# Performance work log

Measured on AMD Instinct MI355X. Metric: run time of the kernel, lower is better.

Reference implementation:

```python
import jax, jax.numpy as jnp
import numpy as np

NUM_USERS = 50000
NUM_FOODS = 20000
USER_FEAT_DIM = 256
FOOD_FEAT_DIM = 256
EMBED_DIM = 128
NUM_LAYERS = 3
NUM_HEADS = 4
THRESHOLD = 0.3
E_UF = 600000  # user->food interactions; symmetrized to 2*E_UF directed edges


def setup_inputs() -> dict:
    key = jax.random.key(0)
    ks = jax.random.split(key, 12)
    user_feat = jax.random.normal(ks[0], (NUM_USERS, USER_FEAT_DIM), jnp.float32)
    food_feat = jax.random.normal(ks[1], (NUM_FOODS, FOOD_FEAT_DIM), jnp.float32)
    # bipartite edges in global index space, symmetrized (both directions)
    u = jax.random.randint(ks[2], (E_UF,), 0, NUM_USERS)
    f = jax.random.randint(ks[3], (E_UF,), 0, NUM_FOODS) + NUM_USERS
    edge_index = jnp.stack([jnp.concatenate([u, f]), jnp.concatenate([f, u])]).astype(jnp.int64)
    s = 0.02
    W_user = jax.random.normal(ks[4], (USER_FEAT_DIM, EMBED_DIM), jnp.float32) * s
    b_user = jnp.zeros((EMBED_DIM,), jnp.float32)
    W_food = jax.random.normal(ks[5], (FOOD_FEAT_DIM, EMBED_DIM), jnp.float32) * s
    b_food = jnp.zeros((EMBED_DIM,), jnp.float32)
    Wq = jax.random.normal(ks[6], (EMBED_DIM, EMBED_DIM), jnp.float32) * s
    Wk = jax.random.normal(ks[7], (EMBED_DIM, EMBED_DIM), jnp.float32) * s
    channel_weights = jnp.zeros((2,), jnp.float32)  # StructurePooling fusion weights
    user_embed = jax.random.normal(ks[8], (NUM_USERS, EMBED_DIM), jnp.float32) * 0.1
    item_embed = jax.random.normal(ks[9], (NUM_FOODS, EMBED_DIM), jnp.float32) * 0.1
    return {"user_feat": user_feat, "food_feat": food_feat, "edge_index": edge_index,
            "W_user": W_user, "b_user": b_user, "W_food": W_food, "b_food": b_food,
            "Wq": Wq, "Wk": Wk, "channel_weights": channel_weights,
            "user_embed": user_embed, "item_embed": item_embed}


def reference(user_feat, food_feat, edge_index, W_user, b_user, W_food, b_food,
              Wq, Wk, channel_weights, user_embed, item_embed):
    N = NUM_USERS + NUM_FOODS
    Dh = EMBED_DIM // NUM_HEADS
    # feature projections + relu
    user_emb = jax.nn.relu(user_feat @ W_user + b_user)   # [U, D]
    food_emb = jax.nn.relu(food_feat @ W_food + b_food)   # [F, D]
    row, col = edge_index[0], edge_index[1]
    # graph generator: per-edge multi-head cosine similarity between user/food endpoints
    u_idx = jnp.where(row < NUM_USERS, row, col)
    f_idx = jnp.where(row < NUM_USERS, col, row) - NUM_USERS
    q = (user_emb[u_idx] @ Wq).reshape(-1, NUM_HEADS, Dh)  # [E, H, Dh]
    k = (food_emb[f_idx] @ Wk).reshape(-1, NUM_HEADS, Dh)
    eps = 1e-8
    sim = (q * k).sum(-1) / (jnp.linalg.norm(q, axis=-1) * jnp.linalg.norm(k, axis=-1) + eps)
    mask_feature = (sim.mean(-1) > THRESHOLD).astype(jnp.float32)  # [E]
    # structure pooling fusion of [all-ones, feature mask]
    w = jax.nn.softmax(channel_weights)
    fused = w[0] * 1.0 + w[1] * mask_feature
    edge_mask = (fused > 0.5).astype(jnp.float32)
    # LightGCN: symmetric-normalized propagation on the masked graph
    deg = jnp.maximum(jax.ops.segment_sum(edge_mask, row, num_segments=N), 1.0)
    norm = edge_mask / jnp.sqrt(deg[row] * deg[col])       # [E]
    x0 = jnp.concatenate([user_embed, item_embed], axis=0)  # [N, D]
    x = x0
    acc = x0
    for _ in range(NUM_LAYERS):
        x = jax.ops.segment_sum(norm[:, None] * x[col], row, num_segments=N)
        acc = acc + x
    out = acc / float(NUM_LAYERS + 1)
    return (out[:NUM_USERS], out[NUM_USERS:], user_embed, item_embed)
```

## Files before the change

kernel.cpp:

```cpp
#include <hip/hip_runtime.h>
#include <cstdint>

#define U_NUM 50000
#define F_NUM 20000
#define N_NUM 70000
#define D_EMB 128
#define THRESH 0.3f

typedef _Float16 half8 __attribute__((ext_vector_type(8)));
typedef float f32x4 __attribute__((ext_vector_type(4)));
typedef unsigned short u16x8 __attribute__((ext_vector_type(8)));

#define NBT_U ((U_NUM + 63) / 64)
#define NBT_F ((F_NUM + 63) / 64)

__device__ __forceinline__ void gl_lds16(const void* g, void* l)
{
    __builtin_amdgcn_global_load_lds(
        (const __attribute__((address_space(1))) unsigned int*)g,
        (__attribute__((address_space(3))) unsigned int*)l, 16, 0, 0);
}

__global__ void presplit_zero(const float* __restrict__ Wu, const float* __restrict__ Wf,
                              const float* __restrict__ Wq, const float* __restrict__ Wk,
                              unsigned short* __restrict__ dst,
                              int* __restrict__ cnt, int* __restrict__ cursor)
{
    int i = blockIdx.x * 256 + threadIdx.x;
    if (i < N_NUM) { cnt[i] = 0; cursor[i] = 0; }
    if (i >= 98304) return;
    float a; size_t d; int pstride;
    if (i < 32768) {
        int n = i >> 8, k = i & 255;
        a = Wu[k * 128 + n]; d = (size_t)n * 256 + k; pstride = 32768;
    } else if (i < 65536) {
        int j = i - 32768; int n = j >> 8, k = j & 255;
        a = Wf[k * 128 + n]; d = 65536 + (size_t)n * 256 + k; pstride = 32768;
    } else if (i < 81920) {
        int j = i - 65536; int n = j >> 7, k = j & 127;
        a = Wq[k * 128 + n]; d = 131072 + (size_t)n * 128 + k; pstride = 16384;
    } else {
        int j = i - 81920; int n = j >> 7, k = j & 127;
        a = Wk[k * 128 + n]; d = 163840 + (size_t)n * 128 + k; pstride = 16384;
    }
    _Float16 c1 = (_Float16)a;
    float r = a - (float)c1;
    _Float16 c2 = (_Float16)r;
    dst[d]           = __builtin_bit_cast(unsigned short, c1);
    dst[d + pstride] = __builtin_bit_cast(unsigned short, c2);
}

__device__ __forceinline__ void split2v(const f32x4 x0, const f32x4 x1,
                                        half8& h, half8& lo)
{
    float v[8] = {x0[0], x0[1], x0[2], x0[3], x1[0], x1[1], x1[2], x1[3]};
#pragma unroll
    for (int i = 0; i < 8; i++) {
        _Float16 c1 = (_Float16)v[i];
        h[i] = c1;
        lo[i] = (_Float16)(v[i] - (float)c1);
    }
}

__global__ __launch_bounds__(256, 2)
void fused_gemm(const float* __restrict__ uf, const float* __restrict__ ff,
                const unsigned short* __restrict__ Wsp,
                const float* __restrict__ bu, const float* __restrict__ bfo,
                float* __restrict__ Qo, unsigned short* __restrict__ QKh)
{
    __shared__ char lds[81920];

    const int bid = blockIdx.x;
    const bool isU = bid < NBT_U;
    const int rt = isU ? bid : bid - NBT_U;
    const int Mloc = isU ? U_NUM : F_NUM;
    const int combBase = isU ? 0 : U_NUM;
    const float* A  = isU ? uf : ff;
    const float* b1 = isU ? bu : bfo;
    const unsigned short* W1 = Wsp + (isU ? 0 : 65536);
    const unsigned short* W2 = Wsp + (isU ? 131072 : 163840);

    const int tid = threadIdx.x;
    const int w  = tid >> 6;
    const int l  = tid & 63;
    const int lm = l & 15;
    const int lq = l >> 4;

    auto stageA = [&](int b, int kc) {
#pragma unroll
        for (int j = 0; j < 2; ++j) {
            int off = j * 4096 + tid * 16;
            int row = off >> 7;
            int ch  = (off & 127) >> 4;
            int gch = ch ^ (row & 7);
            int gr  = min(rt * 64 + row, Mloc - 1);
            const float* src = A + (size_t)gr * 256 + kc * 32 + gch * 4;
            gl_lds16(src, lds + b * 8192 + j * 4096 + w * 1024);
        }
    };
    auto stageW1 = [&](int b, int kc) {
#pragma unroll
        for (int j = 0; j < 4; ++j) {
            int off = w * 4096 + j * 1024 + l * 16;
            int p   = off >> 13;
            int n   = (off & 8191) >> 6;
            int ch  = (off & 63) >> 4;
            int gch = ch ^ ((n >> 1) & 3);
            const unsigned short* src = W1 + (size_t)p * 32768 + (size_t)n * 256 + kc * 32 + gch * 8;
            gl_lds16(src, lds + 16384 + b * 16384 + w * 4096 + j * 1024);
        }
    };
    auto stageW2 = [&](int b, int kc) {
#pragma unroll
        for (int j = 0; j < 4; ++j) {
            int off = w * 4096 + j * 1024 + l * 16;
            int p   = off >> 13;
            int n   = (off & 8191) >> 6;
            int ch  = (off & 63) >> 4;
            int gch = ch ^ ((n >> 1) & 3);
            const unsigned short* src = W2 + (size_t)p * 16384 + (size_t)n * 128 + kc * 32 + gch * 8;
            gl_lds16(src, lds + 16384 + b * 16384 + w * 4096 + j * 1024);
        }
    };

    stageA(0, 0); stageW1(0, 0);
    __syncthreads();

    f32x4 acc1[8];
#pragma unroll
    for (int j = 0; j < 8; j++) acc1[j] = (f32x4)0.f;

    int buf = 0;
#pragma unroll
    for (int kc = 0; kc < 8; ++kc) {
        if (kc < 7) { stageA(buf ^ 1, kc + 1); stageW1(buf ^ 1, kc + 1); }

        half8 ah, al;
        {
            int lr = w * 16 + lm;
            int r7 = lr & 7;
            const float* basep = (const float*)(lds + buf * 8192 + lr * 128);
            f32x4 x0 = *(const f32x4*)(basep + ((((lq * 2)    ) ^ r7) << 2));
            f32x4 x1 = *(const f32x4*)(basep + ((((lq * 2) + 1) ^ r7) << 2));
            split2v(x0, x1, ah, al);
        }
#pragma unroll
        for (int cb = 0; cb < 8; ++cb) {
            int n = cb * 16 + lm;
            int wc = lq ^ ((n >> 1) & 3);
            const char* wbase = lds + 16384 + buf * 16384;
            half8 bh = *(const half8*)(wbase + n * 64 + wc * 16);
            half8 bl = *(const half8*)(wbase + 8192 + n * 64 + wc * 16);
            acc1[cb] = __builtin_amdgcn_mfma_f32_16x16x32_f16(al, bh, acc1[cb], 0, 0, 0);
            acc1[cb] = __builtin_amdgcn_mfma_f32_16x16x32_f16(ah, bl, acc1[cb], 0, 0, 0);
            acc1[cb] = __builtin_amdgcn_mfma_f32_16x16x32_f16(ah, bh, acc1[cb], 0, 0, 0);
        }
        __syncthreads();
        buf ^= 1;
    }

    float* EW = (float*)(lds + 49152 + w * 8192);
#pragma unroll
    for (int cb = 0; cb < 8; ++cb) {
        const int col = cb * 16 + lm;
        const float bb = b1[col];
#pragma unroll
        for (int rg = 0; rg < 4; ++rg) {
            const int row = lq * 4 + rg;
            float e = fmaxf(acc1[cb][rg] + bb, 0.f);
            EW[row * 128 + ((((col >> 2) ^ (row & 7)) << 2) | (col & 3))] = e;
        }
    }

    f32x4 acc2[8];
#pragma unroll
    for (int j = 0; j < 8; j++) acc2[j] = (f32x4)0.f;

    stageW2(0, 0);
    __syncthreads();
    buf = 0;
#pragma unroll
    for (int kc = 0; kc < 4; ++kc) {
        if (kc < 3) stageW2(buf ^ 1, kc + 1);

        half8 ah, al;
        {
            const int row = lm;
            const int r7 = row & 7;
            const int c0 = kc * 8 + lq * 2;
            f32x4 x0 = *(const f32x4*)(EW + row * 128 + (((c0    ) ^ r7) << 2));
            f32x4 x1 = *(const f32x4*)(EW + row * 128 + (((c0 + 1) ^ r7) << 2));
            split2v(x0, x1, ah, al);
        }
#pragma unroll
        for (int cb = 0; cb < 8; ++cb) {
            int n = cb * 16 + lm;
            int wc = lq ^ ((n >> 1) & 3);
            const char* wbase = lds + 16384 + buf * 16384;
            half8 bh = *(const half8*)(wbase + n * 64 + wc * 16);
            half8 bl = *(const half8*)(wbase + 8192 + n * 64 + wc * 16);
            acc2[cb] = __builtin_amdgcn_mfma_f32_16x16x32_f16(al, bh, acc2[cb], 0, 0, 0);
            acc2[cb] = __builtin_amdgcn_mfma_f32_16x16x32_f16(ah, bl, acc2[cb], 0, 0, 0);
            acc2[cb] = __builtin_amdgcn_mfma_f32_16x16x32_f16(ah, bh, acc2[cb], 0, 0, 0);
        }
        __syncthreads();
        buf ^= 1;
    }

#pragma unroll
    for (int cb = 0; cb < 8; ++cb) {
        const int col = cb * 16 + lm;
#pragma unroll
        for (int rg = 0; rg < 4; ++rg) {
            int lr = rt * 64 + w * 16 + lq * 4 + rg;
            if (lr < Mloc) {
                size_t rr = (size_t)(combBase + lr);
                float v = acc2[cb][rg];
                Qo[rr * 128 + col] = v;
                QKh[rr * 128 + col] = __builtin_bit_cast(unsigned short, (_Float16)v);
            }
        }
    }
}

__global__ __launch_bounds__(256)
void edge_kernel(const int* __restrict__ ei, int Edir,
                 const unsigned short* __restrict__ QKh, const float* __restrict__ QKf,
                 const float* __restrict__ cwts,
                 float* __restrict__ maskf, int* __restrict__ cnt, int Eund)
{
    int gid = blockIdx.x * 256 + threadIdx.x;
    int e = gid >> 3;
    if (e >= Eund) return;
    int sub = gid & 7;
    int row = ei[e];
    int col = ei[Edir + e];
    row = min(max(row, 0), N_NUM - 1);
    col = min(max(col, 0), N_NUM - 1);
    int u  = (row < U_NUM) ? row : col;
    int fg = (row < U_NUM) ? col : row;
    u = min(max(u, 0), U_NUM - 1);
    int f = min(max(fg - U_NUM, 0), F_NUM - 1);
    const size_t qrow = (size_t)u * D_EMB;
    const size_t krow = (size_t)(U_NUM + f) * D_EMB;

    const unsigned short* qh = QKh + qrow + sub * 16;
    const unsigned short* kh = QKh + krow + sub * 16;
    u16x8 qa = *(const u16x8*)(qh);
    u16x8 qb = *(const u16x8*)(qh + 8);
    u16x8 ka = *(const u16x8*)(kh);
    u16x8 kb = *(const u16x8*)(kh + 8);
    float dot = 0.f, qq = 0.f, kk = 0.f;
#pragma unroll
    for (int i = 0; i < 8; i++) {
        float qv = (float)__builtin_bit_cast(_Float16, (unsigned short)qa[i]);
        float kv = (float)__builtin_bit_cast(_Float16, (unsigned short)ka[i]);
        dot += qv * kv; qq += qv * qv; kk += kv * kv;
    }
#pragma unroll
    for (int i = 0; i < 8; i++) {
        float qv = (float)__builtin_bit_cast(_Float16, (unsigned short)qb[i]);
        float kv = (float)__builtin_bit_cast(_Float16, (unsigned short)kb[i]);
        dot += qv * kv; qq += qv * qv; kk += kv * kv;
    }
    dot += __shfl_xor(dot, 1);
    qq  += __shfl_xor(qq, 1);
    kk  += __shfl_xor(kk, 1);
    float denom = sqrtf(qq) * sqrtf(kk) + 1e-8f;
    float sim = dot / denom;
    float s = sim + __shfl_xor(sim, 2);
    s += __shfl_xor(s, 4);
    float mean = s * 0.25f;

    if (fabsf(mean - THRESH) < 0.03f) {
        const float4* qp = (const float4*)(QKf + qrow + sub * 16);
        const float4* kp = (const float4*)(QKf + krow + sub * 16);
        float dot2 = 0.f, qq2 = 0.f, kk2 = 0.f;
#pragma unroll
        for (int i = 0; i < 4; i++) {
            float4 a = qp[i]; float4 b = kp[i];
            dot2 += a.x * b.x + a.y * b.y + a.z * b.z + a.w * b.w;
            qq2  += a.x * a.x + a.y * a.y + a.z * a.z + a.w * a.w;
            kk2  += b.x * b.x + b.y * b.y + b.z * b.z + b.w * b.w;
        }
        dot2 += __shfl_xor(dot2, 1);
        qq2  += __shfl_xor(qq2, 1);
        kk2  += __shfl_xor(kk2, 1);
        float denom2 = sqrtf(qq2) * sqrtf(kk2) + 1e-8f;
        float sim2 = dot2 / denom2;
        float s2 = sim2 + __shfl_xor(sim2, 2);
        s2 += __shfl_xor(s2, 4);
        mean = s2 * 0.25f;
    }

    float mf = (mean > THRESH) ? 1.f : 0.f;
    float cw0 = cwts[0], cw1 = cwts[1];
    float mx = fmaxf(cw0, cw1);
    float e0 = expf(cw0 - mx), e1 = expf(cw1 - mx);
    float inv = 1.f / (e0 + e1);
    float fused = e0 * inv + (e1 * inv) * mf;
    float em = (fused > 0.5f) ? 1.f : 0.f;

    if (sub == 0) {
        maskf[e] = em;
        if (em != 0.f) {
            atomicAdd(&cnt[row], 1);
            atomicAdd(&cnt[col], 1);
        }
    }
}

__global__ void scan_part(const int* __restrict__ cnt, int* __restrict__ part, int n)
{
    __shared__ int sd[256];
    int b = blockIdx.x, t = threadIdx.x;
    int base = b * 1024;
    int s = 0;
#pragma unroll
    for (int j = 0; j < 4; j++) {
        int idx = base + t + j * 256;
        if (idx < n) s += cnt[idx];
    }
    sd[t] = s; __syncthreads();
    for (int d = 128; d > 0; d >>= 1) {
        if (t < d) sd[t] += sd[t + d];
        __syncthreads();
    }
    if (t == 0) part[b] = sd[0];
}

__global__ void scan_small(int* part, int nb)
{
    __shared__ int sd[256];
    int t = threadIdx.x;
    sd[t] = (t < nb) ? part[t] : 0;
    __syncthreads();
    for (int d = 1; d < 256; d <<= 1) {
        int x = (t >= d) ? sd[t - d] : 0;
        __syncthreads();
        sd[t] += x;
        __syncthreads();
    }
    if (t < nb) part[t] = (t > 0) ? sd[t - 1] : 0;
}

__global__ void scan_final(const int* __restrict__ cnt, const int* __restrict__ part,
                           int* __restrict__ offs, int n)
{
    __shared__ int sd[256];
    int b = blockIdx.x, t = threadIdx.x;
    int base = b * 1024 + t * 4;
    int v[4]; int s = 0;
#pragma unroll
    for (int j = 0; j < 4; j++) {
        int idx = base + j;
        v[j] = (idx < n) ? cnt[idx] : 0;
        s += v[j];
    }
    sd[t] = s; __syncthreads();
    for (int d = 1; d < 256; d <<= 1) {
        int x = (t >= d) ? sd[t - d] : 0;
        __syncthreads();
        sd[t] += x;
        __syncthreads();
    }
    int prefix = part[b] + ((t > 0) ? sd[t - 1] : 0);
#pragma unroll
    for (int j = 0; j < 4; j++) {
        int idx = base + j;
        if (idx < n) offs[idx] = prefix;
        prefix += v[j];
    }
}

__global__ void scatter_kernel(const int* __restrict__ ei, int Edir,
                               const float* __restrict__ maskf,
                               const int* __restrict__ cnt, const int* __restrict__ offs,
                               int* __restrict__ cursor,
                               int* __restrict__ cnbr, float* __restrict__ cwA, int Eund)
{
    int e = blockIdx.x * 256 + threadIdx.x;
    if (e >= Eund) return;
    if (maskf[e] == 0.f) return;
    int row = ei[e], col = ei[Edir + e];
    row = min(max(row, 0), N_NUM - 1);
    col = min(max(col, 0), N_NUM - 1);
    float w = 1.0f / sqrtf((float)cnt[row] * (float)cnt[col]);
    int p1 = offs[row] + atomicAdd(&cursor[row], 1);
    cnbr[p1] = col; cwA[p1] = w;
    int p2 = offs[col] + atomicAdd(&cursor[col], 1);
    cnbr[p2] = row; cwA[p2] = w;
}

template<int MODE>
__global__ __launch_bounds__(256)
void prop(const int* __restrict__ offs, const int* __restrict__ cnt,
          const int* __restrict__ cnbr, const float* __restrict__ cwA,
          const float* __restrict__ xin,
          const float* __restrict__ ue, const float* __restrict__ ie,
          const float* __restrict__ x1b, float* __restrict__ xout,
          float* __restrict__ tail)
{
    int wid = (blockIdx.x << 2) + (threadIdx.x >> 6);
    if (wid >= N_NUM) return;
    int lane = threadIdx.x & 63;
    int num = cnt[wid];
    if (MODE != 2 && num == 0) return;
    int start = (num > 0) ? offs[wid] : 0;
    float ax = 0.f, ay = 0.f;

    auto srcp = [&](int c) -> const float* {
        if (MODE == 0)
            return (c < U_NUM) ? (ue + (size_t)c * D_EMB) : (ie + (size_t)(c - U_NUM) * D_EMB);
        else
            return xin + (size_t)c * D_EMB;
    };

    int j = 0;
    for (; j + 4 <= num; j += 4) {
        int c0i = cnbr[start + j],     c1i = cnbr[start + j + 1];
        int c2i = cnbr[start + j + 2], c3i = cnbr[start + j + 3];
        float w0 = cwA[start + j],     w1 = cwA[start + j + 1];
        float w2 = cwA[start + j + 2], w3 = cwA[start + j + 3];
        float2 v0 = *(const float2*)(srcp(c0i) + lane * 2);
        float2 v1 = *(const float2*)(srcp(c1i) + lane * 2);
        float2 v2 = *(const float2*)(srcp(c2i) + lane * 2);
        float2 v3 = *(const float2*)(srcp(c3i) + lane * 2);
        ax += w0 * v0.x; ay += w0 * v0.y;
        ax += w1 * v1.x; ay += w1 * v1.y;
        ax += w2 * v2.x; ay += w2 * v2.y;
        ax += w3 * v3.x; ay += w3 * v3.y;
    }
    for (; j < num; ++j) {
        int c = cnbr[start + j]; float w = cwA[start + j];
        float2 v = *(const float2*)(srcp(c) + lane * 2);
        ax += w * v.x; ay += w * v.y;
    }

    size_t o = (size_t)wid * D_EMB + lane * 2;
    if (MODE == 2) {
        const float* x0p = (wid < U_NUM) ? (ue + (size_t)wid * D_EMB)
                                         : (ie + (size_t)(wid - U_NUM) * D_EMB);
        float2 x0v = *(const float2*)(x0p + lane * 2);
        *(float2*)(tail + o) = x0v;
        float ox, oy;
        if (num == 0) {
            ox = x0v.x * 0.25f; oy = x0v.y * 0.25f;
        } else {
            float2 x1v = *(const float2*)(x1b + o);
            float2 x2v = *(const float2*)(xin + o);
            ox = ((x0v.x + x1v.x) + x2v.x + ax) * 0.25f;
            oy = ((x0v.y + x1v.y) + x2v.y + ay) * 0.25f;
        }
        *(float2*)(xout + o) = make_float2(ox, oy);
    } else {
        *(float2*)(xout + o) = make_float2(ax, ay);
    }
}

extern "C" void kernel_launch(void* const* d_in, const int* in_sizes, int n_in,
                              void* d_out, int out_size, void* d_ws, size_t ws_size,
                              hipStream_t stream)
{
    const float* user_feat  = (const float*)d_in[0];
    const float* food_feat  = (const float*)d_in[1];
    const int*   ei         = (const int*)d_in[2];
    const float* W_user     = (const float*)d_in[3];
    const float* b_user     = (const float*)d_in[4];
    const float* W_food     = (const float*)d_in[5];
    const float* b_food     = (const float*)d_in[6];
    const float* Wq         = (const float*)d_in[7];
    const float* Wk         = (const float*)d_in[8];
    const float* cwts       = (const float*)d_in[9];
    const float* user_embed = (const float*)d_in[10];
    const float* item_embed = (const float*)d_in[11];

    const int Edir = in_sizes[2] / 2;
    const int Eund = Edir / 2;

    char* ws = (char*)d_ws;
    size_t off = 0;
    auto alloc = [&](size_t nb) { size_t o = off; off += (nb + 255) & ~(size_t)255; return o; };

    float* Q     = (float*)(ws + alloc((size_t)N_NUM * D_EMB * 4));
    float* xB    = (float*)(ws + alloc((size_t)N_NUM * D_EMB * 4));
    unsigned short* QKh = (unsigned short*)(ws + alloc((size_t)N_NUM * D_EMB * 2));
    float* maskf = (float*)(ws + alloc((size_t)Eund * 4));
    int*   cnt   = (int*)  (ws + alloc((size_t)N_NUM * 4));
    int*   offs  = (int*)  (ws + alloc((size_t)N_NUM * 4));
    int*   cursor= (int*)  (ws + alloc((size_t)N_NUM * 4));
    int*   cnbr  = (int*)  (ws + alloc((size_t)Edir * 4));
    float* cwA   = (float*)(ws + alloc((size_t)Edir * 4));
    int*   part  = (int*)  (ws + alloc((size_t)256 * 4));
    unsigned short* Wsp = (unsigned short*)(ws + alloc((size_t)196608 * 2));
    (void)ws_size; (void)n_in; (void)out_size;

    float* xA = Q;

    presplit_zero<<<384, 256, 0, stream>>>(W_user, W_food, Wq, Wk, Wsp, cnt, cursor);

    fused_gemm<<<NBT_U + NBT_F, 256, 0, stream>>>(user_feat, food_feat, Wsp,
                                                  b_user, b_food, Q, QKh);

    edge_kernel<<<(Eund * 8 + 255) / 256, 256, 0, stream>>>(ei, Edir, QKh, Q, cwts,
                                                            maskf, cnt, Eund);

    int nb = (N_NUM + 1023) / 1024;
    scan_part <<<nb, 256, 0, stream>>>(cnt, part, N_NUM);
    scan_small<<<1, 256, 0, stream>>>(part, nb);
    scan_final<<<nb, 256, 0, stream>>>(cnt, part, offs, N_NUM);

    scatter_kernel<<<(Eund + 255) / 256, 256, 0, stream>>>(ei, Edir, maskf, cnt, offs,
                                                           cursor, cnbr, cwA, Eund);

    int pb = (N_NUM + 3) / 4;
    float* tail = (float*)d_out + (size_t)N_NUM * D_EMB;
    prop<0><<<pb, 256, 0, stream>>>(offs, cnt, cnbr, cwA, nullptr, user_embed, item_embed,
                                    nullptr, xB, nullptr);
    prop<1><<<pb, 256, 0, stream>>>(offs, cnt, cnbr, cwA, xB, user_embed, item_embed,
                                    nullptr, xA, nullptr);
    prop<2><<<pb, 256, 0, stream>>>(offs, cnt, cnbr, cwA, xA, user_embed, item_embed,
                                    xB, (float*)d_out, tail);
}
```

Measured before the change: 129.3 us.

## Shrink GEMM row tile to 32 and split output columns across waves

The fused projection GEMM now handles 32 rows per block instead of 64. Each wave computes a 16-row by 64-column quadrant instead of a 16-row by 128-column slab. The whole 32x256 A tile is loaded into LDS once up front rather than double-buffered per K chunk, and the intermediate ReLU tile is reused in place of A for the second GEMM. LDS drops to 64KB and the grid doubles, aiming for more blocks in flight and fewer accumulator registers. In exchange, the weights are staged twice as often per output row.

```diff
diff --git a/kernel.cpp b/kernel.cpp
--- a/kernel.cpp
+++ b/kernel.cpp
@@ -11,8 +11,8 @@
 typedef float f32x4 __attribute__((ext_vector_type(4)));
 typedef unsigned short u16x8 __attribute__((ext_vector_type(8)));
 
-#define NBT_U ((U_NUM + 63) / 64)
-#define NBT_F ((F_NUM + 63) / 64)
+#define NBT_U ((U_NUM + 31) / 32)
+#define NBT_F ((F_NUM + 31) / 32)
 
 __device__ __forceinline__ void gl_lds16(const void* g, void* l)
 {
@@ -68,7 +68,7 @@
                 const float* __restrict__ bu, const float* __restrict__ bfo,
                 float* __restrict__ Qo, unsigned short* __restrict__ QKh)
 {
-    __shared__ char lds[81920];
+    __shared__ char lds[65536];
 
     const int bid = blockIdx.x;
     const bool isU = bid < NBT_U;
@@ -85,19 +85,22 @@
     const int l  = tid & 63;
     const int lm = l & 15;
     const int lq = l >> 4;
-
-    auto stageA = [&](int b, int kc) {
-#pragma unroll
-        for (int j = 0; j < 2; ++j) {
+    const int rh  = w & 1;
+    const int chf = w >> 1;
+
+    {
+#pragma unroll
+        for (int j = 0; j < 8; ++j) {
             int off = j * 4096 + tid * 16;
-            int row = off >> 7;
-            int ch  = (off & 127) >> 4;
+            int row = off >> 10;
+            int ch  = (off & 1023) >> 4;
             int gch = ch ^ (row & 7);
-            int gr  = min(rt * 64 + row, Mloc - 1);
-            const float* src = A + (size_t)gr * 256 + kc * 32 + gch * 4;
-            gl_lds16(src, lds + b * 8192 + j * 4096 + w * 1024);
-        }
-    };
+            int gr  = min(rt * 32 + row, Mloc - 1);
+            const float* src = A + (size_t)gr * 256 + gch * 4;
+            gl_lds16(src, lds + j * 4096 + w * 1024);
+        }
+    }
+
     auto stageW1 = [&](int b, int kc) {
 #pragma unroll
         for (int j = 0; j < 4; ++j) {
@@ -107,7 +110,7 @@
             int ch  = (off & 63) >> 4;
             int gch = ch ^ ((n >> 1) & 3);
             const unsigned short* src = W1 + (size_t)p * 32768 + (size_t)n * 256 + kc * 32 + gch * 8;
-            gl_lds16(src, lds + 16384 + b * 16384 + w * 4096 + j * 1024);
+            gl_lds16(src, lds + 32768 + b * 16384 + w * 4096 + j * 1024);
         }
     };
     auto stageW2 = [&](int b, int kc) {
@@ -119,36 +122,37 @@
             int ch  = (off & 63) >> 4;
             int gch = ch ^ ((n >> 1) & 3);
             const unsigned short* src = W2 + (size_t)p * 16384 + (size_t)n * 128 + kc * 32 + gch * 8;
-            gl_lds16(src, lds + 16384 + b * 16384 + w * 4096 + j * 1024);
+            gl_lds16(src, lds + 32768 + b * 16384 + w * 4096 + j * 1024);
         }
     };
 
-    stageA(0, 0); stageW1(0, 0);
+    stageW1(0, 0);
     __syncthreads();
 
-    f32x4 acc1[8];
-#pragma unroll
-    for (int j = 0; j < 8; j++) acc1[j] = (f32x4)0.f;
+    f32x4 acc1[4];
+#pragma unroll
+    for (int j = 0; j < 4; j++) acc1[j] = (f32x4)0.f;
 
     int buf = 0;
 #pragma unroll
     for (int kc = 0; kc < 8; ++kc) {
-        if (kc < 7) { stageA(buf ^ 1, kc + 1); stageW1(buf ^ 1, kc + 1); }
+        if (kc < 7) stageW1(buf ^ 1, kc + 1);
 
         half8 ah, al;
         {
-            int lr = w * 16 + lm;
-            int r7 = lr & 7;
-            const float* basep = (const float*)(lds + buf * 8192 + lr * 128);
-            f32x4 x0 = *(const f32x4*)(basep + ((((lq * 2)    ) ^ r7) << 2));
-            f32x4 x1 = *(const f32x4*)(basep + ((((lq * 2) + 1) ^ r7) << 2));
+            int row = rh * 16 + lm;
+            int r7 = row & 7;
+            int c0 = kc * 8 + lq * 2;
+            const float* basep = (const float*)(lds + row * 1024);
+            f32x4 x0 = *(const f32x4*)(basep + (((c0    ) ^ r7) << 2));
+            f32x4 x1 = *(const f32x4*)(basep + (((c0 + 1) ^ r7) << 2));
             split2v(x0, x1, ah, al);
         }
 #pragma unroll
-        for (int cb = 0; cb < 8; ++cb) {
-            int n = cb * 16 + lm;
+        for (int cb = 0; cb < 4; ++cb) {
+            int n = chf * 64 + cb * 16 + lm;
             int wc = lq ^ ((n >> 1) & 3);
-            const char* wbase = lds + 16384 + buf * 16384;
+            const char* wbase = lds + 32768 + buf * 16384;
             half8 bh = *(const half8*)(wbase + n * 64 + wc * 16);
             half8 bl = *(const half8*)(wbase + 8192 + n * 64 + wc * 16);
             acc1[cb] = __builtin_amdgcn_mfma_f32_16x16x32_f16(al, bh, acc1[cb], 0, 0, 0);
@@ -159,25 +163,27 @@
         buf ^= 1;
     }
 
-    float* EW = (float*)(lds + 49152 + w * 8192);
-#pragma unroll
-    for (int cb = 0; cb < 8; ++cb) {
-        const int col = cb * 16 + lm;
-        const float bb = b1[col];
-#pragma unroll
-        for (int rg = 0; rg < 4; ++rg) {
-            const int row = lq * 4 + rg;
-            float e = fmaxf(acc1[cb][rg] + bb, 0.f);
-            EW[row * 128 + ((((col >> 2) ^ (row & 7)) << 2) | (col & 3))] = e;
-        }
-    }
-
-    f32x4 acc2[8];
-#pragma unroll
-    for (int j = 0; j < 8; j++) acc2[j] = (f32x4)0.f;
-
     stageW2(0, 0);
+    {
+        float* E = (float*)lds;
+#pragma unroll
+        for (int cb = 0; cb < 4; ++cb) {
+            const int col = chf * 64 + cb * 16 + lm;
+            const float bb = b1[col];
+#pragma unroll
+            for (int rg = 0; rg < 4; ++rg) {
+                const int row = rh * 16 + lq * 4 + rg;
+                float e = fmaxf(acc1[cb][rg] + bb, 0.f);
+                E[row * 128 + ((((col >> 2) ^ (row & 7)) << 2) | (col & 3))] = e;
+            }
+        }
+    }
     __syncthreads();
+
+    f32x4 acc2[4];
+#pragma unroll
+    for (int j = 0; j < 4; j++) acc2[j] = (f32x4)0.f;
+
     buf = 0;
 #pragma unroll
     for (int kc = 0; kc < 4; ++kc) {
@@ -185,18 +191,19 @@
 
         half8 ah, al;
         {
-            const int row = lm;
+            const int row = rh * 16 + lm;
             const int r7 = row & 7;
             const int c0 = kc * 8 + lq * 2;
-            f32x4 x0 = *(const f32x4*)(EW + row * 128 + (((c0    ) ^ r7) << 2));
-            f32x4 x1 = *(const f32x4*)(EW + row * 128 + (((c0 + 1) ^ r7) << 2));
+            const float* E = (const float*)lds;
+            f32x4 x0 = *(const f32x4*)(E + row * 128 + (((c0    ) ^ r7) << 2));
+            f32x4 x1 = *(const f32x4*)(E + row * 128 + (((c0 + 1) ^ r7) << 2));
             split2v(x0, x1, ah, al);
         }
 #pragma unroll
-        for (int cb = 0; cb < 8; ++cb) {
-            int n = cb * 16 + lm;
+        for (int cb = 0; cb < 4; ++cb) {
+            int n = chf * 64 + cb * 16 + lm;
             int wc = lq ^ ((n >> 1) & 3);
-            const char* wbase = lds + 16384 + buf * 16384;
+            const char* wbase = lds + 32768 + buf * 16384;
             half8 bh = *(const half8*)(wbase + n * 64 + wc * 16);
             half8 bl = *(const half8*)(wbase + 8192 + n * 64 + wc * 16);
             acc2[cb] = __builtin_amdgcn_mfma_f32_16x16x32_f16(al, bh, acc2[cb], 0, 0, 0);
@@ -208,11 +215,11 @@
     }
 
 #pragma unroll
-    for (int cb = 0; cb < 8; ++cb) {
-        const int col = cb * 16 + lm;
+    for (int cb = 0; cb < 4; ++cb) {
+        const int col = chf * 64 + cb * 16 + lm;
 #pragma unroll
         for (int rg = 0; rg < 4; ++rg) {
-            int lr = rt * 64 + w * 16 + lq * 4 + rg;
+            int lr = rt * 32 + rh * 16 + lq * 4 + rg;
             if (lr < Mloc) {
                 size_t rr = (size_t)(combBase + lr);
                 float v = acc2[cb][rg];
```

Result: slower. 133.3 us (+3.0%).

## Use single fp16 GEMMs and recheck near-threshold edges exactly in fp32

Applied to the files above, without the earlier changes.

Replaces the split-fp16 (three MFMA) emulation of fp32 in both projection GEMMs with a single fp16 MFMA per tile, halving weight staging and LDS use. Launch bounds are raised so more blocks fit per CU. The fp32 Q/K output and the in-kernel fp32 recheck are removed. Edges whose fp16 similarity falls within a band of the threshold are pushed to a list, and a new kernel recomputes them from raw features in fp32 and fixes the mask and degree counts. This risks mismatches if fp16 error exceeds the band, and adds per-edge recompute cost proportional to the band population.

```diff
diff --git a/kernel.cpp b/kernel.cpp
--- a/kernel.cpp
+++ b/kernel.cpp
@@ -6,6 +6,7 @@
 #define N_NUM 70000
 #define D_EMB 128
 #define THRESH 0.3f
+#define BAND 0.02f
 
 typedef _Float16 half8 __attribute__((ext_vector_type(8)));
 typedef float f32x4 __attribute__((ext_vector_type(4)));
@@ -24,51 +25,37 @@
 __global__ void presplit_zero(const float* __restrict__ Wu, const float* __restrict__ Wf,
                               const float* __restrict__ Wq, const float* __restrict__ Wk,
                               unsigned short* __restrict__ dst,
-                              int* __restrict__ cnt, int* __restrict__ cursor)
+                              int* __restrict__ cnt, int* __restrict__ cursor,
+                              int* __restrict__ bcount)
 {
     int i = blockIdx.x * 256 + threadIdx.x;
+    if (i == 0) *bcount = 0;
     if (i < N_NUM) { cnt[i] = 0; cursor[i] = 0; }
     if (i >= 98304) return;
-    float a; size_t d; int pstride;
+    float a; size_t d;
     if (i < 32768) {
         int n = i >> 8, k = i & 255;
-        a = Wu[k * 128 + n]; d = (size_t)n * 256 + k; pstride = 32768;
+        a = Wu[k * 128 + n]; d = (size_t)n * 256 + k;
     } else if (i < 65536) {
         int j = i - 32768; int n = j >> 8, k = j & 255;
-        a = Wf[k * 128 + n]; d = 65536 + (size_t)n * 256 + k; pstride = 32768;
+        a = Wf[k * 128 + n]; d = 32768 + (size_t)n * 256 + k;
     } else if (i < 81920) {
         int j = i - 65536; int n = j >> 7, k = j & 127;
-        a = Wq[k * 128 + n]; d = 131072 + (size_t)n * 128 + k; pstride = 16384;
+        a = Wq[k * 128 + n]; d = 65536 + (size_t)n * 128 + k;
     } else {
         int j = i - 81920; int n = j >> 7, k = j & 127;
-        a = Wk[k * 128 + n]; d = 163840 + (size_t)n * 128 + k; pstride = 16384;
-    }
-    _Float16 c1 = (_Float16)a;
-    float r = a - (float)c1;
-    _Float16 c2 = (_Float16)r;
-    dst[d]           = __builtin_bit_cast(unsigned short, c1);
-    dst[d + pstride] = __builtin_bit_cast(unsigned short, c2);
-}
-
-__device__ __forceinline__ void split2v(const f32x4 x0, const f32x4 x1,
-                                        half8& h, half8& lo)
-{
-    float v[8] = {x0[0], x0[1], x0[2], x0[3], x1[0], x1[1], x1[2], x1[3]};
-#pragma unroll
-    for (int i = 0; i < 8; i++) {
-        _Float16 c1 = (_Float16)v[i];
-        h[i] = c1;
-        lo[i] = (_Float16)(v[i] - (float)c1);
-    }
-}
-
-__global__ __launch_bounds__(256, 2)
+        a = Wk[k * 128 + n]; d = 81920 + (size_t)n * 128 + k;
+    }
+    dst[d] = __builtin_bit_cast(unsigned short, (_Float16)a);
+}
+
+__global__ __launch_bounds__(256, 3)
 void fused_gemm(const float* __restrict__ uf, const float* __restrict__ ff,
                 const unsigned short* __restrict__ Wsp,
                 const float* __restrict__ bu, const float* __restrict__ bfo,
-                float* __restrict__ Qo, unsigned short* __restrict__ QKh)
-{
-    __shared__ char lds[81920];
+                unsigned short* __restrict__ QKh)
+{
+    __shared__ char lds[49152];
 
     const int bid = blockIdx.x;
     const bool isU = bid < NBT_U;
@@ -77,8 +64,8 @@
     const int combBase = isU ? 0 : U_NUM;
     const float* A  = isU ? uf : ff;
     const float* b1 = isU ? bu : bfo;
-    const unsigned short* W1 = Wsp + (isU ? 0 : 65536);
-    const unsigned short* W2 = Wsp + (isU ? 131072 : 163840);
+    const unsigned short* W1 = Wsp + (isU ? 0 : 32768);
+    const unsigned short* W2 = Wsp + (isU ? 65536 : 81920);
 
     const int tid = threadIdx.x;
     const int w  = tid >> 6;
@@ -99,31 +86,56 @@
         }
     };
     auto stageW1 = [&](int b, int kc) {
-#pragma unroll
-        for (int j = 0; j < 4; ++j) {
-            int off = w * 4096 + j * 1024 + l * 16;
-            int p   = off >> 13;
-            int n   = (off & 8191) >> 6;
+        {
+            int off = tid * 16;
+        }
+#pragma unroll
+        for (int j = 0; j < 2; ++j) {
+            int off = j * 4096 + tid * 16;
+            int n   = off >> 6;
             int ch  = (off & 63) >> 4;
             int gch = ch ^ ((n >> 1) & 3);
-            const unsigned short* src = W1 + (size_t)p * 32768 + (size_t)n * 256 + kc * 32 + gch * 8;
-            gl_lds16(src, lds + 16384 + b * 16384 + w * 4096 + j * 1024);
+            const unsigned short* src = W1 + (size_t)n * 256 + kc * 32 + gch * 8;
+            gl_lds16(src, lds + 16384 + b * 4096 + j * 4096 + w * 1024);
         }
     };
     auto stageW2 = [&](int b, int kc) {
 #pragma unroll
-        for (int j = 0; j < 4; ++j) {
-            int off = w * 4096 + j * 1024 + l * 16;
-            int p   = off >> 13;
-            int n   = (off & 8191) >> 6;
+        for (int j = 0; j < 2; ++j) {
+            int off = j * 4096 + tid * 16;
+            int n   = off >> 6;
             int ch  = (off & 63) >> 4;
             int gch = ch ^ ((n >> 1) & 3);
-            const unsigned short* src = W2 + (size_t)p * 16384 + (size_t)n * 128 + kc * 32 + gch * 8;
-            gl_lds16(src, lds + 16384 + b * 16384 + w * 4096 + j * 1024);
+            const unsigned short* src = W2 + (size_t)n * 128 + kc * 32 + gch * 8;
+            gl_lds16(src, lds + 16384 + b * 4096 + j * 4096 + w * 1024);
         }
     };
 
-    stageA(0, 0); stageW1(0, 0);
+    (void)stageW1; (void)stageW2;
+    auto stW1 = [&](int b, int kc) {
+#pragma unroll
+        for (int j = 0; j < 2; ++j) {
+            int off = j * 4096 + tid * 16;
+            int n   = off >> 6;
+            int ch  = (off & 63) >> 4;
+            int gch = ch ^ ((n >> 1) & 3);
+            const unsigned short* src = W1 + (size_t)n * 256 + kc * 32 + gch * 8;
+            gl_lds16(src, lds + 16384 + b * 8192 + off - (off & 15));
+        }
+    };
+    auto stW2 = [&](int b, int kc) {
+#pragma unroll
+        for (int j = 0; j < 2; ++j) {
+            int off = j * 4096 + tid * 16;
+            int n   = off >> 6;
+            int ch  = (off & 63) >> 4;
+            int gch = ch ^ ((n >> 1) & 3);
+            const unsigned short* src = W2 + (size_t)n * 128 + kc * 32 + gch * 8;
+            gl_lds16(src, lds + 16384 + b * 8192 + off - (off & 15));
+        }
+    };
+
+    stageA(0, 0); stW1(0, 0);
     __syncthreads();
 
     f32x4 acc1[8];
@@ -133,74 +145,69 @@
     int buf = 0;
 #pragma unroll
     for (int kc = 0; kc < 8; ++kc) {
-        if (kc < 7) { stageA(buf ^ 1, kc + 1); stageW1(buf ^ 1, kc + 1); }
-
-        half8 ah, al;
+        if (kc < 7) { stageA(buf ^ 1, kc + 1); stW1(buf ^ 1, kc + 1); }
+
+        half8 ah;
         {
             int lr = w * 16 + lm;
             int r7 = lr & 7;
             const float* basep = (const float*)(lds + buf * 8192 + lr * 128);
             f32x4 x0 = *(const f32x4*)(basep + ((((lq * 2)    ) ^ r7) << 2));
             f32x4 x1 = *(const f32x4*)(basep + ((((lq * 2) + 1) ^ r7) << 2));
-            split2v(x0, x1, ah, al);
+            float v[8] = {x0[0], x0[1], x0[2], x0[3], x1[0], x1[1], x1[2], x1[3]};
+#pragma unroll
+            for (int i = 0; i < 8; i++) ah[i] = (_Float16)v[i];
         }
 #pragma unroll
         for (int cb = 0; cb < 8; ++cb) {
             int n = cb * 16 + lm;
             int wc = lq ^ ((n >> 1) & 3);
-            const char* wbase = lds + 16384 + buf * 16384;
-            half8 bh = *(const half8*)(wbase + n * 64 + wc * 16);
-            half8 bl = *(const half8*)(wbase + 8192 + n * 64 + wc * 16);
-            acc1[cb] = __builtin_amdgcn_mfma_f32_16x16x32_f16(al, bh, acc1[cb], 0, 0, 0);
-            acc1[cb] = __builtin_amdgcn_mfma_f32_16x16x32_f16(ah, bl, acc1[cb], 0, 0, 0);
+            half8 bh = *(const half8*)(lds + 16384 + buf * 8192 + n * 64 + wc * 16);
             acc1[cb] = __builtin_amdgcn_mfma_f32_16x16x32_f16(ah, bh, acc1[cb], 0, 0, 0);
         }
         __syncthreads();
         buf ^= 1;
     }
 
-    float* EW = (float*)(lds + 49152 + w * 8192);
-#pragma unroll
-    for (int cb = 0; cb < 8; ++cb) {
-        const int col = cb * 16 + lm;
-        const float bb = b1[col];
-#pragma unroll
-        for (int rg = 0; rg < 4; ++rg) {
-            const int row = lq * 4 + rg;
-            float e = fmaxf(acc1[cb][rg] + bb, 0.f);
-            EW[row * 128 + ((((col >> 2) ^ (row & 7)) << 2) | (col & 3))] = e;
-        }
-    }
+    stW2(0, 0);
+    {
+        unsigned short* E = (unsigned short*)(lds + 32768);
+#pragma unroll
+        for (int cb = 0; cb < 8; ++cb) {
+            const int col = cb * 16 + lm;
+            const float bb = b1[col];
+#pragma unroll
+            for (int rg = 0; rg < 4; ++rg) {
+                const int row = w * 16 + lq * 4 + rg;
+                float e = fmaxf(acc1[cb][rg] + bb, 0.f);
+                int chn = (col >> 3) ^ (row & 7);
+                E[row * 128 + chn * 8 + (col & 7)] = __builtin_bit_cast(unsigned short, (_Float16)e);
+            }
+        }
+    }
+    __syncthreads();
 
     f32x4 acc2[8];
 #pragma unroll
     for (int j = 0; j < 8; j++) acc2[j] = (f32x4)0.f;
 
-    stageW2(0, 0);
-    __syncthreads();
     buf = 0;
 #pragma unroll
     for (int kc = 0; kc < 4; ++kc) {
-        if (kc < 3) stageW2(buf ^ 1, kc + 1);
-
-        half8 ah, al;
+        if (kc < 3) stW2(buf ^ 1, kc + 1);
+
+        half8 ah;
         {
-            const int row = lm;
+            const int row = w * 16 + lm;
             const int r7 = row & 7;
-            const int c0 = kc * 8 + lq * 2;
-            f32x4 x0 = *(const f32x4*)(EW + row * 128 + (((c0    ) ^ r7) << 2));
-            f32x4 x1 = *(const f32x4*)(EW + row * 128 + (((c0 + 1) ^ r7) << 2));
-            split2v(x0, x1, ah, al);
+            const int c0 = (kc * 4 + lq) ^ r7;
+            ah = *(const half8*)((const unsigned short*)(lds + 32768) + row * 128 + c0 * 8);
         }
 #pragma unroll
         for (int cb = 0; cb < 8; ++cb) {
             int n = cb * 16 + lm;
             int wc = lq ^ ((n >> 1) & 3);
-            const char* wbase = lds + 16384 + buf * 16384;
-            half8 bh = *(const half8*)(wbase + n * 64 + wc * 16);
-            half8 bl = *(const half8*)(wbase + 8192 + n * 64 + wc * 16);
-            acc2[cb] = __builtin_amdgcn_mfma_f32_16x16x32_f16(al, bh, acc2[cb], 0, 0, 0);
-            acc2[cb] = __builtin_amdgcn_mfma_f32_16x16x32_f16(ah, bl, acc2[cb], 0, 0, 0);
+            half8 bh = *(const half8*)(lds + 16384 + buf * 8192 + n * 64 + wc * 16);
             acc2[cb] = __builtin_amdgcn_mfma_f32_16x16x32_f16(ah, bh, acc2[cb], 0, 0, 0);
         }
         __syncthreads();
@@ -215,9 +222,7 @@
             int lr = rt * 64 + w * 16 + lq * 4 + rg;
             if (lr < Mloc) {
                 size_t rr = (size_t)(combBase + lr);
-                float v = acc2[cb][rg];
-                Qo[rr * 128 + col] = v;
-                QKh[rr * 128 + col] = __builtin_bit_cast(unsigned short, (_Float16)v);
+                QKh[rr * 128 + col] = __builtin_bit_cast(unsigned short, (_Float16)acc2[cb][rg]);
             }
         }
     }
@@ -225,9 +230,10 @@
 
 __global__ __launch_bounds__(256)
 void edge_kernel(const int* __restrict__ ei, int Edir,
-                 const unsigned short* __restrict__ QKh, const float* __restrict__ QKf,
+                 const unsigned short* __restrict__ QKh,
                  const float* __restrict__ cwts,
-                 float* __restrict__ maskf, int* __restrict__ cnt, int Eund)
+                 float* __restrict__ maskf, int* __restrict__ cnt,
+                 int* __restrict__ blist, int* __restrict__ bcount, int Eund)
 {
     int gid = blockIdx.x * 256 + threadIdx.x;
     int e = gid >> 3;
@@ -272,27 +278,6 @@
     s += __shfl_xor(s, 4);
     float mean = s * 0.25f;
 
-    if (fabsf(mean - THRESH) < 0.03f) {
-        const float4* qp = (const float4*)(QKf + qrow + sub * 16);
-        const float4* kp = (const float4*)(QKf + krow + sub * 16);
-        float dot2 = 0.f, qq2 = 0.f, kk2 = 0.f;
-#pragma unroll
-        for (int i = 0; i < 4; i++) {
-            float4 a = qp[i]; float4 b = kp[i];
-            dot2 += a.x * b.x + a.y * b.y + a.z * b.z + a.w * b.w;
-            qq2  += a.x * a.x + a.y * a.y + a.z * a.z + a.w * a.w;
-            kk2  += b.x * b.x + b.y * b.y + b.z * b.z + b.w * b.w;
-        }
-        dot2 += __shfl_xor(dot2, 1);
-        qq2  += __shfl_xor(qq2, 1);
-        kk2  += __shfl_xor(kk2, 1);
-        float denom2 = sqrtf(qq2) * sqrtf(kk2) + 1e-8f;
-        float sim2 = dot2 / denom2;
-        float s2 = sim2 + __shfl_xor(sim2, 2);
-        s2 += __shfl_xor(s2, 4);
-        mean = s2 * 0.25f;
-    }
-
     float mf = (mean > THRESH) ? 1.f : 0.f;
     float cw0 = cwts[0], cw1 = cwts[1];
     float mx = fmaxf(cw0, cw1);
@@ -306,6 +291,109 @@
         if (em != 0.f) {
             atomicAdd(&cnt[row], 1);
             atomicAdd(&cnt[col], 1);
+        }
+        if (fabsf(mean - THRESH) < BAND) {
+            int p = atomicAdd(bcount, 1);
+            blist[p] = e;
+        }
+    }
+}
+
+__global__ __launch_bounds__(256)
+void recheck_kernel(const int* __restrict__ ei, int Edir,
+                    const int* __restrict__ blist, const int* __restrict__ bcount,
+                    const float* __restrict__ uf, const float* __restrict__ ff,
+                    const float* __restrict__ Wu, const float* __restrict__ bu,
+                    const float* __restrict__ Wf, const float* __restrict__ bfo,
+                    const float* __restrict__ Wq, const float* __restrict__ Wk,
+                    const float* __restrict__ cwts,
+                    float* __restrict__ maskf, int* __restrict__ cnt)
+{
+    __shared__ float Esh[4][128];
+    const int w = threadIdx.x >> 6;
+    const int l = threadIdx.x & 63;
+    const int nwaves = gridDim.x * 4;
+    int widx = blockIdx.x * 4 + w;
+    const int total = *bcount;
+
+    for (int i = widx; i < total; i += nwaves) {
+        int e = blist[i];
+        int row = ei[e], col = ei[Edir + e];
+        row = min(max(row, 0), N_NUM - 1);
+        col = min(max(col, 0), N_NUM - 1);
+        int u  = (row < U_NUM) ? row : col;
+        int fg = (row < U_NUM) ? col : row;
+        u = min(max(u, 0), U_NUM - 1);
+        int f = min(max(fg - U_NUM, 0), F_NUM - 1);
+
+        float q0, q1, k0v, k1v;
+        {
+            const float* a = uf + (size_t)u * 256;
+            float e0 = 0.f, e1 = 0.f;
+            for (int k = 0; k < 256; ++k) {
+                float av = a[k];
+                e0 += av * Wu[k * 128 + l];
+                e1 += av * Wu[k * 128 + 64 + l];
+            }
+            e0 = fmaxf(e0 + bu[l], 0.f);
+            e1 = fmaxf(e1 + bu[64 + l], 0.f);
+            Esh[w][l] = e0; Esh[w][64 + l] = e1;
+            float s0 = 0.f, s1 = 0.f;
+            for (int k = 0; k < 128; ++k) {
+                float ev = Esh[w][k];
+                s0 += ev * Wq[k * 128 + l];
+                s1 += ev * Wq[k * 128 + 64 + l];
+            }
+            q0 = s0; q1 = s1;
+        }
+        {
+            const float* a = ff + (size_t)f * 256;
+            float e0 = 0.f, e1 = 0.f;
+            for (int k = 0; k < 256; ++k) {
+                float av = a[k];
+                e0 += av * Wf[k * 128 + l];
+                e1 += av * Wf[k * 128 + 64 + l];
+            }
+            e0 = fmaxf(e0 + bfo[l], 0.f);
+            e1 = fmaxf(e1 + bfo[64 + l], 0.f);
+            Esh[w][l] = e0; Esh[w][64 + l] = e1;
+            float s0 = 0.f, s1 = 0.f;
+            for (int k = 0; k < 128; ++k) {
+                float ev = Esh[w][k];
+                s0 += ev * Wk[k * 128 + l];
+                s1 += ev * Wk[k * 128 + 64 + l];
+            }
+            k0v = s0; k1v = s1;
+        }
+        float d0 = q0 * k0v, d1 = q1 * k1v;
+        float qa = q0 * q0, qb = q1 * q1, ka = k0v * k0v, kb = k1v * k1v;
+#pragma unroll
+        for (int off = 1; off < 32; off <<= 1) {
+            d0 += __shfl_xor(d0, off); d1 += __shfl_xor(d1, off);
+            qa += __shfl_xor(qa, off); qb += __shfl_xor(qb, off);
+            ka += __shfl_xor(ka, off); kb += __shfl_xor(kb, off);
+        }
+        float sA = d0 / (sqrtf(qa) * sqrtf(ka) + 1e-8f);
+        float sB = d1 / (sqrtf(qb) * sqrtf(kb) + 1e-8f);
+        float s = sA + sB;
+        s += __shfl_xor(s, 32);
+        float mean = s * 0.25f;
+
+        if (l == 0) {
+            float mf = (mean > THRESH) ? 1.f : 0.f;
+            float cw0 = cwts[0], cw1 = cwts[1];
+            float mx = fmaxf(cw0, cw1);
+            float e0 = expf(cw0 - mx), e1 = expf(cw1 - mx);
+            float inv = 1.f / (e0 + e1);
+            float fusedv = e0 * inv + (e1 * inv) * mf;
+            bool em = fusedv > 0.5f;
+            bool old = maskf[e] > 0.5f;
+            if (em != old) {
+                maskf[e] = em ? 1.f : 0.f;
+                int d = em ? 1 : -1;
+                atomicAdd(&cnt[row], d);
+                atomicAdd(&cnt[col], d);
+            }
         }
     }
 }
@@ -482,7 +570,7 @@
     size_t off = 0;
     auto alloc = [&](size_t nb) { size_t o = off; off += (nb + 255) & ~(size_t)255; return o; };
 
-    float* Q     = (float*)(ws + alloc((size_t)N_NUM * D_EMB * 4));
+    float* xA    = (float*)(ws + alloc((size_t)N_NUM * D_EMB * 4));
     float* xB    = (float*)(ws + alloc((size_t)N_NUM * D_EMB * 4));
     unsigned short* QKh = (unsigned short*)(ws + alloc((size_t)N_NUM * D_EMB * 2));
     float* maskf = (float*)(ws + alloc((size_t)Eund * 4));
@@ -492,18 +580,23 @@
     int*   cnbr  = (int*)  (ws + alloc((size_t)Edir * 4));
     float* cwA   = (float*)(ws + alloc((size_t)Edir * 4));
     int*   part  = (int*)  (ws + alloc((size_t)256 * 4));
-    unsigned short* Wsp = (unsigned short*)(ws + alloc((size_t)196608 * 2));
+    unsigned short* Wsp = (unsigned short*)(ws + alloc((size_t)98304 * 2));
+    int*   blist = (int*)  (ws + alloc((size_t)Eund * 4));
+    int*   bcount= (int*)  (ws + alloc(256));
     (void)ws_size; (void)n_in; (void)out_size;
 
-    float* xA = Q;
-
-    presplit_zero<<<384, 256, 0, stream>>>(W_user, W_food, Wq, Wk, Wsp, cnt, cursor);
+    presplit_zero<<<384, 256, 0, stream>>>(W_user, W_food, Wq, Wk, Wsp, cnt, cursor, bcount);
 
     fused_gemm<<<NBT_U + NBT_F, 256, 0, stream>>>(user_feat, food_feat, Wsp,
-                                                  b_user, b_food, Q, QKh);
-
-    edge_kernel<<<(Eund * 8 + 255) / 256, 256, 0, stream>>>(ei, Edir, QKh, Q, cwts,
-                                                            maskf, cnt, Eund);
+                                                  b_user, b_food, QKh);
+
+    edge_kernel<<<(Eund * 8 + 255) / 256, 256, 0, stream>>>(ei, Edir, QKh, cwts,
+                                                            maskf, cnt, blist, bcount, Eund);
+
+    recheck_kernel<<<1024, 256, 0, stream>>>(ei, Edir, blist, bcount,
+                                             user_feat, food_feat,
+                                             W_user, b_user, W_food, b_food,
+                                             Wq, Wk, cwts, maskf, cnt);
 
     int nb = (N_NUM + 1023) / 1024;
     scan_part <<<nb, 256, 0, stream>>>(cnt, part, N_NUM);
```

New measurement: 136.9 us. +5.8%, slower.
